# Optimization experiments

Measured on AMD Instinct MI355X. Metric: run time of the kernel, lower is better.

## Reference

```python
import jax, jax.numpy as jnp
import numpy as np

D = 128          # feature / hidden dim
K = 3            # SortPooling k (hard-coded in Topkpool)
NUM_CLASS = 10
EPS = 1e-5       # BatchNorm eps


def setup_inputs() -> dict:
    key = jax.random.key(0)
    ks = jax.random.split(key, 24)
    G, NPG = 512, 200
    N = G * NPG
    E = 1638400
    inp = {
        "x": jax.random.normal(ks[0], (N, D), jnp.float32),
        "src": jax.random.randint(ks[1], (E,), 0, N),
        "dst": jax.random.randint(ks[2], (E,), 0, N),
        "num_graphs": G,
        "nodes_per_graph": NPG,
    }
    s = 1.0 / np.sqrt(D)
    for i in (1, 2, 3):
        inp[f"W{i}"] = jax.random.uniform(ks[2 + i], (D, D), jnp.float32, -s, s)
        inp[f"b{i}"] = jnp.zeros((D,), jnp.float32)
        inp[f"g{i}"] = jnp.ones((D,), jnp.float32)   # BN gamma
        inp[f"bt{i}"] = jnp.zeros((D,), jnp.float32)  # BN beta
    sp = 1.0 / np.sqrt(K * D)
    for i in range(4):
        inp[f"P{i}w"] = jax.random.uniform(ks[10 + i], (K * D, NUM_CLASS), jnp.float32, -sp, sp)
        inp[f"P{i}b"] = jnp.zeros((NUM_CLASS,), jnp.float32)
    return inp


def _graph_conv(h, src, dst, W, b, n):
    # DGL GraphConv, norm='both': D_in^{-1/2} A (D_out^{-1/2} h) W + b
    one = jnp.ones((src.shape[0],), h.dtype)
    deg_out = jnp.zeros((n,), h.dtype).at[src].add(one)
    deg_in = jnp.zeros((n,), h.dtype).at[dst].add(one)
    h = h * jax.lax.rsqrt(jnp.maximum(deg_out, 1.0))[:, None]
    agg = jax.ops.segment_sum(h[src], dst, num_segments=n)  # [N, D] scatter-add
    agg = agg * jax.lax.rsqrt(jnp.maximum(deg_in, 1.0))[:, None]
    return agg @ W + b


def _bn_relu(h, g, bt):
    mu = h.mean(axis=0)
    var = jnp.mean((h - mu) ** 2, axis=0)  # biased var, torch BN training mode
    return jax.nn.relu((h - mu) * jax.lax.rsqrt(var + EPS) * g + bt)


def _sort_pool(h, G, npg):
    # DGL SortPooling: sort each node's feature vector ascending, then pick
    # top-K nodes per graph by last (max) channel, concatenate features.
    d = h.shape[-1]
    hs = jnp.sort(h, axis=-1).reshape(G, npg, d)
    idx = jax.lax.top_k(hs[:, :, -1], K)[1]                       # [G, K]
    return jnp.take_along_axis(hs, idx[:, :, None], axis=1).reshape(G, K * d)


def reference(x, W1, b1, g1, bt1, W2, b2, g2, bt2, W3, b3, g3, bt3,
              P0w, P0b, P1w, P1b, P2w, P2b, P3w, P3b,
              src, dst, num_graphs, nodes_per_graph):
    n = x.shape[0]
    reps = [x]
    h = x
    for W, b, g, bt in ((W1, b1, g1, bt1), (W2, b2, g2, bt2), (W3, b3, g3, bt3)):
        h = _bn_relu(_graph_conv(h, src, dst, W, b, n), g, bt)
        reps.append(h)
    score = jnp.zeros((num_graphs, NUM_CLASS), x.dtype)
    for h_i, Pw, Pb in zip(reps, (P0w, P1w, P2w, P3w), (P0b, P1b, P2b, P3b)):
        score = score + _sort_pool(h_i, num_graphs, nodes_per_graph) @ Pw + Pb
    return score
```

## Files before the change

kernel.cpp:

```cpp
#include <hip/hip_runtime.h>
#include <hip/hip_bf16.h>

#define D 128
#define KTOP 3
#define NCLS 10
#define EPS 1e-5f
#define GBM 128
#define BCAP 64


__global__ __launch_bounds__(256) void prologue_kernel(
        const int* __restrict__ src,
        int* __restrict__ deg_out, int E,
        const float* __restrict__ x, float* __restrict__ nodemax, int N,
        float* __restrict__ score, const float* __restrict__ pb0,
        const float* __restrict__ pb1, const float* __restrict__ pb2,
        const float* __restrict__ pb3, int G) {
    int b = blockIdx.x;
    int nbDeg = (E + 255) >> 8;
    if (b < nbDeg) {
        int e = b * 256 + threadIdx.x;
        if (e < E) atomicAdd(&deg_out[src[e]], 1);
        return;
    }
    b -= nbDeg;
    int nbR = N >> 3;
    if (b < nbR) {
        int node = b * 8 + (threadIdx.x >> 5);
        int l = threadIdx.x & 31;
        float4 v = *reinterpret_cast<const float4*>(x + (size_t)node * D + 4 * l);
        float m = fmaxf(fmaxf(v.x, v.y), fmaxf(v.z, v.w));
#pragma unroll
        for (int d = 16; d > 0; d >>= 1) m = fmaxf(m, __shfl_xor(m, d, 64));
        if (l == 0) nodemax[node] = m;
        return;
    }
    for (int i = threadIdx.x; i < G * NCLS; i += 256) {
        int c = i % NCLS;
        score[i] = pb0[c] + pb1[c] + pb2[c] + pb3[c];
    }
}

__global__ void rs_out_kernel(const int* __restrict__ deg_out,
                              float* __restrict__ rs_out, int N) {
    int i = blockIdx.x * blockDim.x + threadIdx.x;
    if (i >= N) return;
    int a = deg_out[i]; if (a < 1) a = 1;
    rs_out[i] = rsqrtf((float)a);
}

__global__ void csr_scatter(const int* __restrict__ src, const int* __restrict__ dst,
                            const float* __restrict__ rs_out,
                            int* __restrict__ cursor, int2* __restrict__ csrw, int E) {
    int e = blockIdx.x * blockDim.x + threadIdx.x;
    if (e >= E) return;
    int d = dst[e], s = src[e];
    int slot = atomicAdd(&cursor[d], 1);
    if (slot >= BCAP) return;
    int2 p; p.x = s; p.y = __float_as_int(rs_out[s]);
    csrw[(size_t)d * BCAP + slot] = p;
}

__global__ void pad_kernel(const int* __restrict__ cursor, int2* __restrict__ csrw, int N) {
    int d = blockIdx.x * blockDim.x + threadIdx.x;
    if (d >= N) return;
    int c = cursor[d]; if (c > BCAP) c = BCAP;
    int end = (c + 7) & ~7;
    int2 z; z.x = 0; z.y = 0;
    for (int i = c; i < end; ++i) csrw[(size_t)d * BCAP + i] = z;
}


__global__ __launch_bounds__(256) void aggregate_kernel(const float* __restrict__ hin,
        const int* __restrict__ cursor, const int2* __restrict__ csrw,
        float* __restrict__ hout, int N) {
    int node = (blockIdx.x * 256 + threadIdx.x) >> 5;
    int l = threadIdx.x & 31;
    if (node >= N) return;
    int deg = cursor[node];
    int end = (deg + 7) & ~7;
    const int2* bkt = csrw + (size_t)node * BCAP;
    const float* base = hin + 4 * l;
    float4 a0 = {0.f, 0.f, 0.f, 0.f}, a1 = a0;
    for (int e = 0; e < end; e += 8) {
        const int4* ce = reinterpret_cast<const int4*>(bkt + e);
        int4 p0 = ce[0], p1 = ce[1], p2 = ce[2], p3 = ce[3];
        float4 v0 = *reinterpret_cast<const float4*>(base + (size_t)p0.x * D);
        float4 v1 = *reinterpret_cast<const float4*>(base + (size_t)p0.z * D);
        float4 v2 = *reinterpret_cast<const float4*>(base + (size_t)p1.x * D);
        float4 v3 = *reinterpret_cast<const float4*>(base + (size_t)p1.z * D);
        float4 v4 = *reinterpret_cast<const float4*>(base + (size_t)p2.x * D);
        float4 v5 = *reinterpret_cast<const float4*>(base + (size_t)p2.z * D);
        float4 v6 = *reinterpret_cast<const float4*>(base + (size_t)p3.x * D);
        float4 v7 = *reinterpret_cast<const float4*>(base + (size_t)p3.z * D);
        float w0 = __int_as_float(p0.y), w1 = __int_as_float(p0.w);
        float w2 = __int_as_float(p1.y), w3 = __int_as_float(p1.w);
        float w4 = __int_as_float(p2.y), w5 = __int_as_float(p2.w);
        float w6 = __int_as_float(p3.y), w7 = __int_as_float(p3.w);
        a0.x += w0*v0.x; a0.y += w0*v0.y; a0.z += w0*v0.z; a0.w += w0*v0.w;
        a1.x += w1*v1.x; a1.y += w1*v1.y; a1.z += w1*v1.z; a1.w += w1*v1.w;
        a0.x += w2*v2.x; a0.y += w2*v2.y; a0.z += w2*v2.z; a0.w += w2*v2.w;
        a1.x += w3*v3.x; a1.y += w3*v3.y; a1.z += w3*v3.z; a1.w += w3*v3.w;
        a0.x += w4*v4.x; a0.y += w4*v4.y; a0.z += w4*v4.z; a0.w += w4*v4.w;
        a1.x += w5*v5.x; a1.y += w5*v5.y; a1.z += w5*v5.z; a1.w += w5*v5.w;
        a0.x += w6*v6.x; a0.y += w6*v6.y; a0.z += w6*v6.z; a0.w += w6*v6.w;
        a1.x += w7*v7.x; a1.y += w7*v7.y; a1.z += w7*v7.z; a1.w += w7*v7.w;
    }
    float ri = rsqrtf((float)(deg < 1 ? 1 : deg));
    float4 r;
    r.x = (a0.x + a1.x) * ri;
    r.y = (a0.y + a1.y) * ri;
    r.z = (a0.z + a1.z) * ri;
    r.w = (a0.w + a1.w) * ri;
    *reinterpret_cast<float4*>(hout + (size_t)node * D + 4 * l) = r;
}


__device__ __forceinline__ void gemm_chunk(const float* __restrict__ ain, size_t rowBase,
        int kc, int c0, const float (*Wl)[D], float (&acc)[4][8]) {
#pragma unroll 2
    for (int k4 = 0; k4 < 16; ++k4) {
        const float* ap = ain + rowBase * D + kc + 4 * k4;
        float4 a0 = *reinterpret_cast<const float4*>(ap);
        float4 a1 = *reinterpret_cast<const float4*>(ap + D);
        float4 a2 = *reinterpret_cast<const float4*>(ap + 2 * D);
        float4 a3 = *reinterpret_cast<const float4*>(ap + 3 * D);
#pragma unroll
        for (int j = 0; j < 4; ++j) {
            int kk = 4 * k4 + j;
            float4 w0 = *reinterpret_cast<const float4*>(&Wl[kk][c0]);
            float4 w1 = *reinterpret_cast<const float4*>(&Wl[kk][c0 + 4]);
            float av[4];
            av[0] = (j==0)?a0.x:(j==1)?a0.y:(j==2)?a0.z:a0.w;
            av[1] = (j==0)?a1.x:(j==1)?a1.y:(j==2)?a1.z:a1.w;
            av[2] = (j==0)?a2.x:(j==1)?a2.y:(j==2)?a2.z:a2.w;
            av[3] = (j==0)?a3.x:(j==1)?a3.y:(j==2)?a3.z:a3.w;
            float wv[8] = {w0.x, w0.y, w0.z, w0.w, w1.x, w1.y, w1.z, w1.w};
#pragma unroll
            for (int i = 0; i < 4; ++i)
#pragma unroll
                for (int jj = 0; jj < 8; ++jj) acc[i][jj] += av[i] * wv[jj];
        }
    }
}

__global__ __launch_bounds__(512) void gemm_bn(const float* __restrict__ ain,
        const float* __restrict__ W, const float* __restrict__ bias,
        float* __restrict__ hout, float* __restrict__ bnsums, int N) {
    __shared__ __align__(16) float Wl[64][D];
    int t = threadIdx.x;
    int cg = t & 15;
    int rs = t >> 4;
    int c0 = cg * 8;
    size_t rowBase = (size_t)blockIdx.x * GBM + 4 * rs;

    float acc[4][8];
#pragma unroll
    for (int i = 0; i < 4; ++i)
#pragma unroll
        for (int j = 0; j < 8; ++j) acc[i][j] = 0.f;

    const float4* Wv = reinterpret_cast<const float4*>(W);
    float4* Wd = reinterpret_cast<float4*>(&Wl[0][0]);
    float4 wpre[4];
#pragma unroll
    for (int i = 0; i < 4; ++i) wpre[i] = Wv[t + 512 * i];
#pragma unroll
    for (int i = 0; i < 4; ++i) Wd[t + 512 * i] = wpre[i];
#pragma unroll
    for (int i = 0; i < 4; ++i) wpre[i] = Wv[2048 + t + 512 * i];
    __syncthreads();
    gemm_chunk(ain, rowBase, 0, c0, Wl, acc);
    __syncthreads();
#pragma unroll
    for (int i = 0; i < 4; ++i) Wd[t + 512 * i] = wpre[i];
    __syncthreads();
    gemm_chunk(ain, rowBase, 64, c0, Wl, acc);

    float4 b0 = *reinterpret_cast<const float4*>(&bias[c0]);
    float4 b1 = *reinterpret_cast<const float4*>(&bias[c0 + 4]);
    float bv[8] = {b0.x, b0.y, b0.z, b0.w, b1.x, b1.y, b1.z, b1.w};
    float cs[8], cq[8];
#pragma unroll
    for (int j = 0; j < 8; ++j) { cs[j] = 0.f; cq[j] = 0.f; }
#pragma unroll
    for (int i = 0; i < 4; ++i) {
#pragma unroll
        for (int j = 0; j < 8; ++j) {
            float v = acc[i][j] + bv[j];
            acc[i][j] = v;
            cs[j] += v;
            cq[j] += v * v;
        }
    }
#pragma unroll
    for (int i = 0; i < 4; ++i) {
        size_t row = rowBase + i;
        float4 o0, o1;
        o0.x = acc[i][0]; o0.y = acc[i][1]; o0.z = acc[i][2]; o0.w = acc[i][3];
        o1.x = acc[i][4]; o1.y = acc[i][5]; o1.z = acc[i][6]; o1.w = acc[i][7];
        *reinterpret_cast<float4*>(&hout[row * D + c0])     = o0;
        *reinterpret_cast<float4*>(&hout[row * D + c0 + 4]) = o1;
    }
#pragma unroll
    for (int j = 0; j < 8; ++j) {
        cs[j] += __shfl_xor(cs[j], 16, 64); cq[j] += __shfl_xor(cq[j], 16, 64);
        cs[j] += __shfl_xor(cs[j], 32, 64); cq[j] += __shfl_xor(cq[j], 32, 64);
    }
    __syncthreads();
    float* red = &Wl[0][0];
    int wid = t >> 6, lane = t & 63;
    if (lane < 16) {
#pragma unroll
        for (int j = 0; j < 8; ++j) {
            red[wid * 256 + lane * 16 + j]     = cs[j];
            red[wid * 256 + lane * 16 + 8 + j] = cq[j];
        }
    }
    __syncthreads();
    if (t < 256) {
        float s = 0.f;
#pragma unroll
        for (int w = 0; w < 8; ++w) s += red[w * 256 + t];
        int cgi = t >> 4, r = t & 15;
        int ch = cgi * 8 + (r & 7);
        atomicAdd(&bnsums[(r < 8 ? 0 : D) + ch], s);
    }
}


__global__ void bn_final(const float* __restrict__ sums, const float* __restrict__ g,
                         const float* __restrict__ bt, float* __restrict__ sc,
                         float* __restrict__ sh, int N) {
    int c = threadIdx.x;
    if (c >= D) return;
    float mu  = sums[c] / (float)N;
    float var = sums[D + c] / (float)N - mu * mu;
    float inv = rsqrtf(var + EPS);
    float scale = g[c] * inv;
    sc[c] = scale;
    sh[c] = bt[c] - mu * scale;
}

__global__ __launch_bounds__(256) void bn_apply_relu_max(float* __restrict__ h,
        const float* __restrict__ sc, const float* __restrict__ sh,
        float* __restrict__ nodemax, int N) {
    int node = (blockIdx.x * 256 + threadIdx.x) >> 5;
    int l = threadIdx.x & 31;
    if (node >= N) return;
    float4 v = *reinterpret_cast<const float4*>(h + (size_t)node * D + 4 * l);
    float4 a = *reinterpret_cast<const float4*>(sc + 4 * l);
    float4 b = *reinterpret_cast<const float4*>(sh + 4 * l);
    v.x = fmaxf(fmaf(v.x, a.x, b.x), 0.f);
    v.y = fmaxf(fmaf(v.y, a.y, b.y), 0.f);
    v.z = fmaxf(fmaf(v.z, a.z, b.z), 0.f);
    v.w = fmaxf(fmaf(v.w, a.w, b.w), 0.f);
    *reinterpret_cast<float4*>(h + (size_t)node * D + 4 * l) = v;
    float m = fmaxf(fmaxf(v.x, v.y), fmaxf(v.z, v.w));
#pragma unroll
    for (int d = 16; d > 0; d >>= 1) m = fmaxf(m, __shfl_xor(m, d, 64));
    if (l == 0) nodemax[node] = m;
}


__global__ __launch_bounds__(384) void topk_sort_head(
        const float* __restrict__ feat, const float* __restrict__ nodemax,
        const float* __restrict__ Pw, float* __restrict__ score, int NPG) {
    int g = blockIdx.x;
    int t = threadIdx.x;
    __shared__ float ov[256];
    __shared__ float sv[256];
    __shared__ int   si[256];
    __shared__ int   sel[KTOP];
    __shared__ float sbuf[KTOP][D];
    __shared__ float red[6][NCLS];
    if (t < 256) ov[t] = (t < NPG) ? nodemax[(size_t)g * NPG + t] : -3.4e38f;
    __syncthreads();
    for (int ks = 0; ks < KTOP; ++ks) {
        if (t < 256) { sv[t] = ov[t]; si[t] = t; }
        __syncthreads();
        for (int s = 128; s > 0; s >>= 1) {
            if (t < s) {
                float a = sv[t], b = sv[t + s];
                int ia = si[t], ib = si[t + s];
                if (b > a || (b == a && ib < ia)) { sv[t] = b; si[t] = ib; }
            }
            __syncthreads();
        }
        if (t == 0) { sel[ks] = si[0]; ov[si[0]] = -3.4e38f; }
        __syncthreads();
    }
    int u = t >> 7, tl = t & 127;
    size_t node = (size_t)g * NPG + sel[u];
    sbuf[u][tl] = feat[node * D + tl];
    __syncthreads();
    for (int size = 2; size <= D; size <<= 1) {
        for (int stride = size >> 1; stride > 0; stride >>= 1) {
            int ixj = tl ^ stride;
            if (ixj > tl) {
                float a = sbuf[u][tl], c = sbuf[u][ixj];
                bool up = ((tl & size) == 0);
                if ((a > c) == up) { sbuf[u][tl] = c; sbuf[u][ixj] = a; }
            }
            __syncthreads();
        }
    }
    float v = sbuf[u][tl];
    const float* pw = Pw + (size_t)(u * D + tl) * NCLS;
    float part[NCLS];
#pragma unroll
    for (int c = 0; c < NCLS; ++c) part[c] = v * pw[c];
    int lane = t & 63, wid = t >> 6;
#pragma unroll
    for (int c = 0; c < NCLS; ++c) {
        float x = part[c];
#pragma unroll
        for (int o = 32; o > 0; o >>= 1) x += __shfl_down(x, o, 64);
        if (lane == 0) red[wid][c] = x;
    }
    __syncthreads();
    if (t < NCLS) {
        float s = red[0][t] + red[1][t] + red[2][t] +
                  red[3][t] + red[4][t] + red[5][t];
        atomicAdd(&score[g * NCLS + t], s);
    }
}


extern "C" void kernel_launch(void* const* d_in, const int* in_sizes, int n_in,
                              void* d_out, int out_size, void* d_ws, size_t ws_size,
                              hipStream_t stream) {
    const float* x   = (const float*)d_in[0];
    const int*   src = (const int*)d_in[1];
    const int*   dst = (const int*)d_in[2];
    const float* W[3]  = {(const float*)d_in[5],  (const float*)d_in[9],  (const float*)d_in[13]};
    const float* bb[3] = {(const float*)d_in[6],  (const float*)d_in[10], (const float*)d_in[14]};
    const float* gg[3] = {(const float*)d_in[7],  (const float*)d_in[11], (const float*)d_in[15]};
    const float* bt[3] = {(const float*)d_in[8],  (const float*)d_in[12], (const float*)d_in[16]};
    const float* Pw[4] = {(const float*)d_in[17], (const float*)d_in[19], (const float*)d_in[21], (const float*)d_in[23]};
    const float* Pb[4] = {(const float*)d_in[18], (const float*)d_in[20], (const float*)d_in[22], (const float*)d_in[24]};

    int N = in_sizes[0] / D;
    int E = in_sizes[1];
    int G = out_size / NCLS;
    int NPG = N / G;
    float* score = (float*)d_out;

    size_t NF = (size_t)N * D;
    float* fws     = (float*)d_ws;
    float* H       = fws;
    float* T       = H + NF;
    float* rs_out  = T + NF;
    float* nodemax = rs_out + N;
    float* bnsums  = nodemax + N;
    float* bscale  = bnsums + 6 * D;
    float* bshift  = bscale + D;
    int* deg_out = (int*)(bshift + D);
    int* cursor  = deg_out + N;
    int2* csrw   = (int2*)(cursor + N + 2);

    int nbDeg = (E + 255) >> 8;
    int nbR = N >> 3;

    hipMemsetAsync(deg_out, 0, sizeof(int) * (size_t)2 * N, stream);
    hipMemsetAsync(bnsums, 0, sizeof(float) * 6 * D, stream);

    prologue_kernel<<<nbDeg + nbR + 1, 256, 0, stream>>>(
        src, deg_out, E, x, nodemax, N,
        score, Pb[0], Pb[1], Pb[2], Pb[3], G);
    rs_out_kernel<<<(N + 255) / 256, 256, 0, stream>>>(deg_out, rs_out, N);
    csr_scatter<<<(E + 255) / 256, 256, 0, stream>>>(src, dst, rs_out, cursor, csrw, E);
    pad_kernel<<<(N + 255) / 256, 256, 0, stream>>>(cursor, csrw, N);

    topk_sort_head<<<G, 384, 0, stream>>>(x, nodemax, Pw[0], score, NPG);

    const float* hin = x;
    for (int l = 0; l < 3; ++l) {
        float* bns = bnsums + l * 2 * D;
        aggregate_kernel<<<N / 8, 256, 0, stream>>>(hin, cursor, csrw, T, N);
        gemm_bn<<<N / GBM, 512, 0, stream>>>(T, W[l], bb[l], H, bns, N);
        bn_final<<<1, D, 0, stream>>>(bns, gg[l], bt[l], bscale, bshift, N);
        bn_apply_relu_max<<<N / 8, 256, 0, stream>>>(H, bscale, bshift, nodemax, N);
        topk_sort_head<<<G, 384, 0, stream>>>(H, nodemax, Pw[l + 1], score, NPG);
        hin = H;
    }
}
```

Before: 858.7 us.

## Fuse top-k sort-pool head into column-split aggregation and fold BN finalize

Aggregation is split into two column halves, each handled by 16 lanes per node. The sort-pool head blocks for the previous layer are appended to the same launch, so they run alongside the aggregation, and the head now uses 256 threads instead of 384. The BN scale/shift finalize is folded into the apply kernel, which removes one tiny launch per layer. This cuts launch count and lets the head overlap with gather work. The risk is worse gather locality from the half-row split, plus redundant per-block BN finalize computation.

```diff
diff --git a/kernel.cpp b/kernel.cpp
--- a/kernel.cpp
+++ b/kernel.cpp
@@ -71,48 +71,128 @@
 }
 
 
-__global__ __launch_bounds__(256) void aggregate_kernel(const float* __restrict__ hin,
-        const int* __restrict__ cursor, const int2* __restrict__ csrw,
-        float* __restrict__ hout, int N) {
-    int node = (blockIdx.x * 256 + threadIdx.x) >> 5;
-    int l = threadIdx.x & 31;
-    if (node >= N) return;
-    int deg = cursor[node];
-    int end = (deg + 7) & ~7;
-    const int2* bkt = csrw + (size_t)node * BCAP;
-    const float* base = hin + 4 * l;
-    float4 a0 = {0.f, 0.f, 0.f, 0.f}, a1 = a0;
-    for (int e = 0; e < end; e += 8) {
-        const int4* ce = reinterpret_cast<const int4*>(bkt + e);
-        int4 p0 = ce[0], p1 = ce[1], p2 = ce[2], p3 = ce[3];
-        float4 v0 = *reinterpret_cast<const float4*>(base + (size_t)p0.x * D);
-        float4 v1 = *reinterpret_cast<const float4*>(base + (size_t)p0.z * D);
-        float4 v2 = *reinterpret_cast<const float4*>(base + (size_t)p1.x * D);
-        float4 v3 = *reinterpret_cast<const float4*>(base + (size_t)p1.z * D);
-        float4 v4 = *reinterpret_cast<const float4*>(base + (size_t)p2.x * D);
-        float4 v5 = *reinterpret_cast<const float4*>(base + (size_t)p2.z * D);
-        float4 v6 = *reinterpret_cast<const float4*>(base + (size_t)p3.x * D);
-        float4 v7 = *reinterpret_cast<const float4*>(base + (size_t)p3.z * D);
-        float w0 = __int_as_float(p0.y), w1 = __int_as_float(p0.w);
-        float w2 = __int_as_float(p1.y), w3 = __int_as_float(p1.w);
-        float w4 = __int_as_float(p2.y), w5 = __int_as_float(p2.w);
-        float w6 = __int_as_float(p3.y), w7 = __int_as_float(p3.w);
-        a0.x += w0*v0.x; a0.y += w0*v0.y; a0.z += w0*v0.z; a0.w += w0*v0.w;
-        a1.x += w1*v1.x; a1.y += w1*v1.y; a1.z += w1*v1.z; a1.w += w1*v1.w;
-        a0.x += w2*v2.x; a0.y += w2*v2.y; a0.z += w2*v2.z; a0.w += w2*v2.w;
-        a1.x += w3*v3.x; a1.y += w3*v3.y; a1.z += w3*v3.z; a1.w += w3*v3.w;
-        a0.x += w4*v4.x; a0.y += w4*v4.y; a0.z += w4*v4.z; a0.w += w4*v4.w;
-        a1.x += w5*v5.x; a1.y += w5*v5.y; a1.z += w5*v5.z; a1.w += w5*v5.w;
-        a0.x += w6*v6.x; a0.y += w6*v6.y; a0.z += w6*v6.z; a0.w += w6*v6.w;
-        a1.x += w7*v7.x; a1.y += w7*v7.y; a1.z += w7*v7.z; a1.w += w7*v7.w;
-    }
-    float ri = rsqrtf((float)(deg < 1 ? 1 : deg));
-    float4 r;
-    r.x = (a0.x + a1.x) * ri;
-    r.y = (a0.y + a1.y) * ri;
-    r.z = (a0.z + a1.z) * ri;
-    r.w = (a0.w + a1.w) * ri;
-    *reinterpret_cast<float4*>(hout + (size_t)node * D + 4 * l) = r;
+__global__ __launch_bounds__(256) void aggregate_head(
+        const float* __restrict__ hin, const int* __restrict__ cursor,
+        const int2* __restrict__ csrw, float* __restrict__ hout, int nHalf,
+        const float* __restrict__ nodemax, const float* __restrict__ Pw,
+        float* __restrict__ score, int NPG) {
+    __shared__ float ov[256];
+    __shared__ float sv[256];
+    __shared__ int   si[256];
+    __shared__ int   sel[KTOP];
+    __shared__ float sbuf[KTOP][D];
+    __shared__ float red[4][NCLS];
+    int b = blockIdx.x;
+    int t = threadIdx.x;
+    int nAgg = 2 * nHalf;
+    if (b < nAgg) {
+        int pass = (b >= nHalf) ? 1 : 0;
+        int nb = pass ? b - nHalf : b;
+        int node = nb * 16 + (t >> 4);
+        int l = t & 15;
+        int colOff = (pass << 6) + 4 * l;
+        int deg = cursor[node];
+        int end = (deg + 7) & ~7;
+        const int2* bkt = csrw + (size_t)node * BCAP;
+        const float* base = hin + colOff;
+        float4 a0 = {0.f, 0.f, 0.f, 0.f}, a1 = a0;
+        for (int e = 0; e < end; e += 8) {
+            const int4* ce = reinterpret_cast<const int4*>(bkt + e);
+            int4 p0 = ce[0], p1 = ce[1], p2 = ce[2], p3 = ce[3];
+            float4 v0 = *reinterpret_cast<const float4*>(base + (size_t)p0.x * D);
+            float4 v1 = *reinterpret_cast<const float4*>(base + (size_t)p0.z * D);
+            float4 v2 = *reinterpret_cast<const float4*>(base + (size_t)p1.x * D);
+            float4 v3 = *reinterpret_cast<const float4*>(base + (size_t)p1.z * D);
+            float4 v4 = *reinterpret_cast<const float4*>(base + (size_t)p2.x * D);
+            float4 v5 = *reinterpret_cast<const float4*>(base + (size_t)p2.z * D);
+            float4 v6 = *reinterpret_cast<const float4*>(base + (size_t)p3.x * D);
+            float4 v7 = *reinterpret_cast<const float4*>(base + (size_t)p3.z * D);
+            float w0 = __int_as_float(p0.y), w1 = __int_as_float(p0.w);
+            float w2 = __int_as_float(p1.y), w3 = __int_as_float(p1.w);
+            float w4 = __int_as_float(p2.y), w5 = __int_as_float(p2.w);
+            float w6 = __int_as_float(p3.y), w7 = __int_as_float(p3.w);
+            a0.x += w0*v0.x; a0.y += w0*v0.y; a0.z += w0*v0.z; a0.w += w0*v0.w;
+            a1.x += w1*v1.x; a1.y += w1*v1.y; a1.z += w1*v1.z; a1.w += w1*v1.w;
+            a0.x += w2*v2.x; a0.y += w2*v2.y; a0.z += w2*v2.z; a0.w += w2*v2.w;
+            a1.x += w3*v3.x; a1.y += w3*v3.y; a1.z += w3*v3.z; a1.w += w3*v3.w;
+            a0.x += w4*v4.x; a0.y += w4*v4.y; a0.z += w4*v4.z; a0.w += w4*v4.w;
+            a1.x += w5*v5.x; a1.y += w5*v5.y; a1.z += w5*v5.z; a1.w += w5*v5.w;
+            a0.x += w6*v6.x; a0.y += w6*v6.y; a0.z += w6*v6.z; a0.w += w6*v6.w;
+            a1.x += w7*v7.x; a1.y += w7*v7.y; a1.z += w7*v7.z; a1.w += w7*v7.w;
+        }
+        float ri = rsqrtf((float)(deg < 1 ? 1 : deg));
+        float4 r;
+        r.x = (a0.x + a1.x) * ri;
+        r.y = (a0.y + a1.y) * ri;
+        r.z = (a0.z + a1.z) * ri;
+        r.w = (a0.w + a1.w) * ri;
+        *reinterpret_cast<float4*>(hout + (size_t)node * D + colOff) = r;
+        return;
+    }
+
+    int gr = b - nAgg;
+    ov[t] = (t < NPG) ? nodemax[(size_t)gr * NPG + t] : -3.4e38f;
+    __syncthreads();
+    for (int ks = 0; ks < KTOP; ++ks) {
+        sv[t] = ov[t]; si[t] = t;
+        __syncthreads();
+        for (int s = 128; s > 0; s >>= 1) {
+            if (t < s) {
+                float a = sv[t], c = sv[t + s];
+                int ia = si[t], ib = si[t + s];
+                if (c > a || (c == a && ib < ia)) { sv[t] = c; si[t] = ib; }
+            }
+            __syncthreads();
+        }
+        if (t == 0) { sel[ks] = si[0]; ov[si[0]] = -3.4e38f; }
+        __syncthreads();
+    }
+    int u = t >> 7, tl = t & 127;
+    sbuf[u][tl] = hin[((size_t)gr * NPG + sel[u]) * D + tl];
+    if (t < 128) sbuf[2][t] = hin[((size_t)gr * NPG + sel[2]) * D + t];
+    __syncthreads();
+    for (int size = 2; size <= D; size <<= 1) {
+        for (int stride = size >> 1; stride > 0; stride >>= 1) {
+            int ixj = tl ^ stride;
+            if (ixj > tl) {
+                float a = sbuf[u][tl], c = sbuf[u][ixj];
+                bool up = ((tl & size) == 0);
+                if ((a > c) == up) { sbuf[u][tl] = c; sbuf[u][ixj] = a; }
+            }
+            if (t < 128) {
+                int ix2 = t ^ stride;
+                if (ix2 > t) {
+                    float a = sbuf[2][t], c = sbuf[2][ix2];
+                    bool up = ((t & size) == 0);
+                    if ((a > c) == up) { sbuf[2][t] = c; sbuf[2][ix2] = a; }
+                }
+            }
+            __syncthreads();
+        }
+    }
+    float part[NCLS];
+    float v0 = sbuf[u][tl];
+    const float* pw0 = Pw + (size_t)(u * D + tl) * NCLS;
+#pragma unroll
+    for (int c = 0; c < NCLS; ++c) part[c] = v0 * pw0[c];
+    if (t < 128) {
+        float v2 = sbuf[2][t];
+        const float* pw2 = Pw + (size_t)(2 * D + t) * NCLS;
+#pragma unroll
+        for (int c = 0; c < NCLS; ++c) part[c] += v2 * pw2[c];
+    }
+    int lane = t & 63, wid = t >> 6;
+#pragma unroll
+    for (int c = 0; c < NCLS; ++c) {
+        float xx = part[c];
+#pragma unroll
+        for (int o = 32; o > 0; o >>= 1) xx += __shfl_down(xx, o, 64);
+        if (lane == 0) red[wid][c] = xx;
+    }
+    __syncthreads();
+    if (t < NCLS)
+        atomicAdd(&score[gr * NCLS + t],
+                  red[0][t] + red[1][t] + red[2][t] + red[3][t]);
 }
 
 
@@ -229,28 +309,26 @@
 }
 
 
-__global__ void bn_final(const float* __restrict__ sums, const float* __restrict__ g,
-                         const float* __restrict__ bt, float* __restrict__ sc,
-                         float* __restrict__ sh, int N) {
-    int c = threadIdx.x;
-    if (c >= D) return;
-    float mu  = sums[c] / (float)N;
-    float var = sums[D + c] / (float)N - mu * mu;
-    float inv = rsqrtf(var + EPS);
-    float scale = g[c] * inv;
-    sc[c] = scale;
-    sh[c] = bt[c] - mu * scale;
-}
-
 __global__ __launch_bounds__(256) void bn_apply_relu_max(float* __restrict__ h,
-        const float* __restrict__ sc, const float* __restrict__ sh,
-        float* __restrict__ nodemax, int N) {
-    int node = (blockIdx.x * 256 + threadIdx.x) >> 5;
-    int l = threadIdx.x & 31;
+        const float* __restrict__ bnsums, const float* __restrict__ g,
+        const float* __restrict__ bt, float* __restrict__ nodemax, int N, float invN) {
+    __shared__ float sc[D], sh[D];
+    int t = threadIdx.x;
+    if (t < D) {
+        float mu  = bnsums[t] * invN;
+        float var = bnsums[D + t] * invN - mu * mu;
+        float inv = rsqrtf(var + EPS);
+        float s = g[t] * inv;
+        sc[t] = s;
+        sh[t] = bt[t] - mu * s;
+    }
+    __syncthreads();
+    int node = (blockIdx.x * 256 + t) >> 5;
+    int l = t & 31;
     if (node >= N) return;
     float4 v = *reinterpret_cast<const float4*>(h + (size_t)node * D + 4 * l);
-    float4 a = *reinterpret_cast<const float4*>(sc + 4 * l);
-    float4 b = *reinterpret_cast<const float4*>(sh + 4 * l);
+    float4 a = *reinterpret_cast<const float4*>(&sc[4 * l]);
+    float4 b = *reinterpret_cast<const float4*>(&sh[4 * l]);
     v.x = fmaxf(fmaf(v.x, a.x, b.x), 0.f);
     v.y = fmaxf(fmaf(v.y, a.y, b.y), 0.f);
     v.z = fmaxf(fmaf(v.z, a.z, b.z), 0.f);
@@ -260,70 +338,6 @@
 #pragma unroll
     for (int d = 16; d > 0; d >>= 1) m = fmaxf(m, __shfl_xor(m, d, 64));
     if (l == 0) nodemax[node] = m;
-}
-
-
-__global__ __launch_bounds__(384) void topk_sort_head(
-        const float* __restrict__ feat, const float* __restrict__ nodemax,
-        const float* __restrict__ Pw, float* __restrict__ score, int NPG) {
-    int g = blockIdx.x;
-    int t = threadIdx.x;
-    __shared__ float ov[256];
-    __shared__ float sv[256];
-    __shared__ int   si[256];
-    __shared__ int   sel[KTOP];
-    __shared__ float sbuf[KTOP][D];
-    __shared__ float red[6][NCLS];
-    if (t < 256) ov[t] = (t < NPG) ? nodemax[(size_t)g * NPG + t] : -3.4e38f;
-    __syncthreads();
-    for (int ks = 0; ks < KTOP; ++ks) {
-        if (t < 256) { sv[t] = ov[t]; si[t] = t; }
-        __syncthreads();
-        for (int s = 128; s > 0; s >>= 1) {
-            if (t < s) {
-                float a = sv[t], b = sv[t + s];
-                int ia = si[t], ib = si[t + s];
-                if (b > a || (b == a && ib < ia)) { sv[t] = b; si[t] = ib; }
-            }
-            __syncthreads();
-        }
-        if (t == 0) { sel[ks] = si[0]; ov[si[0]] = -3.4e38f; }
-        __syncthreads();
-    }
-    int u = t >> 7, tl = t & 127;
-    size_t node = (size_t)g * NPG + sel[u];
-    sbuf[u][tl] = feat[node * D + tl];
-    __syncthreads();
-    for (int size = 2; size <= D; size <<= 1) {
-        for (int stride = size >> 1; stride > 0; stride >>= 1) {
-            int ixj = tl ^ stride;
-            if (ixj > tl) {
-                float a = sbuf[u][tl], c = sbuf[u][ixj];
-                bool up = ((tl & size) == 0);
-                if ((a > c) == up) { sbuf[u][tl] = c; sbuf[u][ixj] = a; }
-            }
-            __syncthreads();
-        }
-    }
-    float v = sbuf[u][tl];
-    const float* pw = Pw + (size_t)(u * D + tl) * NCLS;
-    float part[NCLS];
-#pragma unroll
-    for (int c = 0; c < NCLS; ++c) part[c] = v * pw[c];
-    int lane = t & 63, wid = t >> 6;
-#pragma unroll
-    for (int c = 0; c < NCLS; ++c) {
-        float x = part[c];
-#pragma unroll
-        for (int o = 32; o > 0; o >>= 1) x += __shfl_down(x, o, 64);
-        if (lane == 0) red[wid][c] = x;
-    }
-    __syncthreads();
-    if (t < NCLS) {
-        float s = red[0][t] + red[1][t] + red[2][t] +
-                  red[3][t] + red[4][t] + red[5][t];
-        atomicAdd(&score[g * NCLS + t], s);
-    }
 }
 
 
@@ -353,14 +367,13 @@
     float* rs_out  = T + NF;
     float* nodemax = rs_out + N;
     float* bnsums  = nodemax + N;
-    float* bscale  = bnsums + 6 * D;
-    float* bshift  = bscale + D;
-    int* deg_out = (int*)(bshift + D);
+    int* deg_out = (int*)(bnsums + 6 * D);
     int* cursor  = deg_out + N;
-    int2* csrw   = (int2*)(cursor + N + 2);
+    int2* csrw   = (int2*)(cursor + N);
 
     int nbDeg = (E + 255) >> 8;
     int nbR = N >> 3;
+    float invN = 1.0f / (float)N;
 
     hipMemsetAsync(deg_out, 0, sizeof(int) * (size_t)2 * N, stream);
     hipMemsetAsync(bnsums, 0, sizeof(float) * 6 * D, stream);
@@ -372,16 +385,16 @@
     csr_scatter<<<(E + 255) / 256, 256, 0, stream>>>(src, dst, rs_out, cursor, csrw, E);
     pad_kernel<<<(N + 255) / 256, 256, 0, stream>>>(cursor, csrw, N);
 
-    topk_sort_head<<<G, 384, 0, stream>>>(x, nodemax, Pw[0], score, NPG);
-
+    int nHalf = N / 16;
     const float* hin = x;
     for (int l = 0; l < 3; ++l) {
         float* bns = bnsums + l * 2 * D;
-        aggregate_kernel<<<N / 8, 256, 0, stream>>>(hin, cursor, csrw, T, N);
+        aggregate_head<<<2 * nHalf + G, 256, 0, stream>>>(
+            hin, cursor, csrw, T, nHalf, nodemax, Pw[l], score, NPG);
         gemm_bn<<<N / GBM, 512, 0, stream>>>(T, W[l], bb[l], H, bns, N);
-        bn_final<<<1, D, 0, stream>>>(bns, gg[l], bt[l], bscale, bshift, N);
-        bn_apply_relu_max<<<N / 8, 256, 0, stream>>>(H, bscale, bshift, nodemax, N);
-        topk_sort_head<<<G, 384, 0, stream>>>(H, nodemax, Pw[l + 1], score, NPG);
+        bn_apply_relu_max<<<N / 8, 256, 0, stream>>>(H, bns, gg[l], bt[l], nodemax, N, invN);
         hin = H;
     }
-}
+    aggregate_head<<<G, 256, 0, stream>>>(
+        H, cursor, csrw, T, 0, nodemax, Pw[3], score, NPG);
+}
```

Result: faster. 830.7 us (-3.3%).
